# Performance work log

Measured on AMD Instinct MI355X. Metric: run time of the kernel, lower is better.

The kernel has to match this reference:

```python
import jax, jax.numpy as jnp
import numpy as np

NUM_CHANNELS = 512
B_DIM = 64
C_DIM = 16
N = 512
FEAT = NUM_CHANNELS * 4 * 4  # 8192


def setup_inputs() -> dict:
    key = jax.random.key(0)
    k1, k2 = jax.random.split(key)
    inp = jax.random.normal(k1, (N, NUM_CHANNELS, 4, 4), dtype=jnp.float32)
    T = jax.random.normal(k2, (FEAT, B_DIM * C_DIM), dtype=jnp.float32) * 0.1
    return {"inp": inp, "T": T}


def reference(inp, T):
    x = inp.reshape(-1, FEAT)                      # (N, 8192)
    M = (x @ T).reshape(-1, B_DIM, C_DIM)          # (N, B, C)
    # pairwise L1 distance over C: (N, N, B)
    dist = jnp.sum(jnp.abs(M[:, None, :, :] - M[None, :, :, :]), axis=-1)
    o = jnp.sum(jnp.exp(-dist), axis=1)            # (N, B)
    return jnp.concatenate((x, o), axis=1)         # (N, 8192 + B)
```

## Files before the change

### kernel.cpp

```cpp
#include <hip/hip_runtime.h>

#define NROWS 512
#define FEAT  8192
#define BDIM  64
#define CDIM  16
#define MCOLS 1024
#define OUTC  8256
#define KSPLIT 8
#define KCHUNK (FEAT / KSPLIT)
#define MSIZE  (NROWS * MCOLS)

typedef __bf16 bf16x8 __attribute__((ext_vector_type(8)));
typedef float  floatx4 __attribute__((ext_vector_type(4)));

#define AS1 __attribute__((address_space(1)))
#define AS3 __attribute__((address_space(3)))

static __device__ __forceinline__ void gload16(const void* g, void* l) {
    __builtin_amdgcn_global_load_lds((AS1 void*)(g), (AS3 void*)(l), 16, 0, 0);
}

static __device__ __forceinline__ unsigned short f2bf(float f) {
    unsigned int x = __builtin_bit_cast(unsigned int, f);
    unsigned int r = (x + 0x7FFFu + ((x >> 16) & 1u)) >> 16;
    return (unsigned short)r;
}

__global__ __launch_bounds__(512, 2) void k_prep(const float* __restrict__ x,
                                                 const float* __restrict__ T,
                                                 unsigned short* __restrict__ xb,
                                                 unsigned short* __restrict__ Tt,
                                                 float* __restrict__ out) {
    __shared__ __align__(16) float lds[2][64][65];
    int bid = blockIdx.x, t = threadIdx.x;
#pragma unroll
    for (int u = 0; u < 8; ++u) {
        int gid = bid * 4096 + u * 512 + t;
        float4 v = *(const float4*)(x + (size_t)gid * 4);
        ushort4 uu;
        uu.x = f2bf(v.x); uu.y = f2bf(v.y); uu.z = f2bf(v.z); uu.w = f2bf(v.w);
        *(ushort4*)(xb + (size_t)gid * 4) = uu;
        int row = gid >> 11, col4 = gid & 2047;
        *(float4*)(out + (size_t)row * OUTC + col4 * 4) = v;
    }
    int sub = t >> 8, tt = t & 255;
    for (int u = 0; u < 4; ++u) {
        int tile = bid * 8 + u * 2 + sub;
        int kt = tile & 127, nt = tile >> 7;
        __syncthreads();
        int kk = tt >> 2, q = tt & 3;
#pragma unroll
        for (int p = 0; p < 4; ++p) {
            int c4 = q + p * 4;
            float4 v = *(const float4*)(T + (size_t)(kt * 64 + kk) * MCOLS + nt * 64 + c4 * 4);
            lds[sub][kk][c4 * 4 + 0] = v.x; lds[sub][kk][c4 * 4 + 1] = v.y;
            lds[sub][kk][c4 * 4 + 2] = v.z; lds[sub][kk][c4 * 4 + 3] = v.w;
        }
        __syncthreads();
        int nr = tt >> 2, ck = tt & 3;
        unsigned int wv[8];
#pragma unroll
        for (int j = 0; j < 8; ++j) {
            unsigned int lo = f2bf(lds[sub][ck * 16 + j * 2 + 0][nr]);
            unsigned int hi = f2bf(lds[sub][ck * 16 + j * 2 + 1][nr]);
            wv[j] = lo | (hi << 16);
        }
        uint4* dst = (uint4*)(Tt + (size_t)(nt * 64 + nr) * FEAT + kt * 64 + ck * 16);
        dst[0] = make_uint4(wv[0], wv[1], wv[2], wv[3]);
        dst[1] = make_uint4(wv[4], wv[5], wv[6], wv[7]);
    }
}

__global__ __launch_bounds__(256, 2) void k_gemm(const unsigned short* __restrict__ xb,
                                                 const unsigned short* __restrict__ Tt,
                                                 float* __restrict__ Mp) {
    __shared__ __align__(16) unsigned short ldsA[128 * 64];
    __shared__ __align__(16) unsigned short ldsB[64 * 64];
    int bid = blockIdx.x, t = threadIdx.x;
    int mt = bid & 3, nt = (bid >> 2) & 15, ks = bid >> 6;
    int m0 = mt * 128, n0 = nt * 64, kbase = ks * KCHUNK;
    int w = t >> 6, l = t & 63;

    int c  = (l & 3) ^ ((l >> 3) & 3);
    int lr = l >> 2;
    const unsigned short* gA0 = xb + (size_t)(m0 + w * 32 + lr) * FEAT + kbase + c * 8;
    const unsigned short* gA1 = gA0 + (size_t)16 * FEAT;
    const unsigned short* gB0 = Tt + (size_t)(n0 + w * 16 + lr) * FEAT + kbase + c * 8;
    unsigned short* lA00 = ldsA + (4 * w + 0) * 512;
    unsigned short* lA01 = ldsA + (4 * w + 1) * 512;
    unsigned short* lA10 = ldsA + (4 * w + 2) * 512;
    unsigned short* lA11 = ldsA + (4 * w + 3) * 512;
    unsigned short* lB0  = ldsB + (2 * w + 0) * 512;
    unsigned short* lB1  = ldsB + (2 * w + 1) * 512;

    int wr = w >> 1, wc = w & 1, fm = l & 15, fq = l >> 4;
    int fo = fm * 32 + ((fq ^ ((fm >> 1) & 3)) * 8);
    const unsigned short* paB = ldsA + (wr * 8) * 512 + fo;
    const unsigned short* pbB = ldsB + (wc * 4) * 512 + fo;

    floatx4 acc[4][2] = {};

    for (int kk = 0; kk < KCHUNK; kk += 64) {
        __syncthreads();
        gload16(gA0 + kk,      lA00);
        gload16(gA0 + kk + 32, lA01);
        gload16(gA1 + kk,      lA10);
        gload16(gA1 + kk + 32, lA11);
        gload16(gB0 + kk,      lB0);
        gload16(gB0 + kk + 32, lB1);
        __syncthreads();
#pragma unroll
        for (int h = 0; h < 2; ++h) {
            bf16x8 af[4], bfr[2];
#pragma unroll
            for (int a = 0; a < 4; ++a) af[a]  = *(const bf16x8*)(paB + (a * 2 + h) * 512);
#pragma unroll
            for (int b = 0; b < 2; ++b) bfr[b] = *(const bf16x8*)(pbB + (b * 2 + h) * 512);
#pragma unroll
            for (int a = 0; a < 4; ++a)
#pragma unroll
                for (int b = 0; b < 2; ++b)
                    acc[a][b] = __builtin_amdgcn_mfma_f32_16x16x32_bf16(af[a], bfr[b], acc[a][b], 0, 0, 0);
        }
    }

    float* outp = Mp + (size_t)ks * MSIZE;
    int gr0 = m0 + wr * 64, gc0 = n0 + wc * 32;
#pragma unroll
    for (int a = 0; a < 4; ++a)
#pragma unroll
        for (int r = 0; r < 4; ++r) {
            int row = gr0 + a * 16 + fq * 4 + r;
#pragma unroll
            for (int b = 0; b < 2; ++b)
                outp[(size_t)row * MCOLS + gc0 + b * 16 + fm] = acc[a][b][r];
        }
}

__global__ __launch_bounds__(512, 2) void k_pair(const float* __restrict__ Mp,
                                                 float* __restrict__ out) {
    __shared__ float ldsM[NROWS * 20];
    __shared__ float partial[8][64];
    int bid = blockIdx.x, t = threadIdx.x;
    int b = bid & 63, itp = bid >> 6;
#pragma unroll
    for (int p = 0; p < 4; ++p) {
        int idx = t + p * 512;
        int j = idx >> 2, c4 = idx & 3;
        const float* base = Mp + (size_t)j * MCOLS + b * CDIM + c4 * 4;
        float4 s = *(const float4*)base;
#pragma unroll
        for (int k = 1; k < KSPLIT; ++k) {
            float4 v = *(const float4*)(base + (size_t)k * MSIZE);
            s.x += v.x; s.y += v.y; s.z += v.z; s.w += v.w;
        }
        *(float4*)&ldsM[j * 20 + c4 * 4] = s;
    }
    __syncthreads();

    int lane = t & 63, w = t >> 6, g = t >> 8, wg = (t >> 6) & 3;
    int i = (itp * 2 + g) * 64 + lane;
    float mi[CDIM];
#pragma unroll
    for (int cc = 0; cc < CDIM; ++cc) mi[cc] = ldsM[i * 20 + cc];

    float acc = 0.0f;
    for (int jj = wg * 128; jj < wg * 128 + 128; ++jj) {
        float d = 0.0f;
#pragma unroll
        for (int cc = 0; cc < CDIM; ++cc) d += fabsf(mi[cc] - ldsM[jj * 20 + cc]);
        acc += __expf(-d);
    }
    partial[w][lane] = acc;
    __syncthreads();
    if ((t & 255) < 64) {
        int ii = (itp * 2 + g) * 64 + (t & 63);
        float o = partial[g * 4 + 0][t & 63] + partial[g * 4 + 1][t & 63] +
                  partial[g * 4 + 2][t & 63] + partial[g * 4 + 3][t & 63];
        out[(size_t)ii * OUTC + FEAT + b] = o;
    }
}

extern "C" void kernel_launch(void* const* d_in, const int* in_sizes, int n_in,
                              void* d_out, int out_size, void* d_ws, size_t ws_size,
                              hipStream_t stream) {
    const float* x = (const float*)d_in[0];
    const float* T = (const float*)d_in[1];
    float* out = (float*)d_out;

    unsigned short* xb = (unsigned short*)d_ws;
    unsigned short* Tt = (unsigned short*)((char*)d_ws + (8u << 20));
    float*          Mp = (float*)((char*)d_ws + (24u << 20));

    k_prep<<<256, 512, 0, stream>>>(x, T, xb, Tt, out);
    k_gemm<<<512, 256, 0, stream>>>(xb, Tt, Mp);
    k_pair<<<256, 512, 0, stream>>>(Mp, out);
}
```

Baseline: 136.0 us.

## Use packed fp16 L1 distances in pair kernel and split prep into separate blocks

The pairwise kernel now stores the reduced M rows as packed fp16 in shared memory and computes the L1 distance with packed half2 subtract, abs and add. This cuts LDS traffic and ALU work in the O(N^2·B) inner loop. The cost is reduced precision in the distances before exp, which may hurt accuracy. Separately, the prep kernel launches twice as many blocks so x conversion and T transposition run in different blocks instead of sequentially in the same block.

Result: no change. 137.9 us (+1.4%).

```diff
diff --git a/kernel.cpp b/kernel.cpp
--- a/kernel.cpp
+++ b/kernel.cpp
@@ -12,6 +12,7 @@
 
 typedef __bf16 bf16x8 __attribute__((ext_vector_type(8)));
 typedef float  floatx4 __attribute__((ext_vector_type(4)));
+typedef _Float16 half2 __attribute__((ext_vector_type(2)));
 
 #define AS1 __attribute__((address_space(1)))
 #define AS3 __attribute__((address_space(3)))
@@ -24,6 +25,15 @@
     unsigned int x = __builtin_bit_cast(unsigned int, f);
     unsigned int r = (x + 0x7FFFu + ((x >> 16) & 1u)) >> 16;
     return (unsigned short)r;
+}
+
+static __device__ __forceinline__ unsigned int pk2h(float a, float b) {
+    return __builtin_bit_cast(unsigned int, __builtin_amdgcn_cvt_pkrtz(a, b));
+}
+
+static __device__ __forceinline__ half2 absdiff2(unsigned int a, unsigned int b) {
+    half2 d = __builtin_bit_cast(half2, a) - __builtin_bit_cast(half2, b);
+    return __builtin_bit_cast(half2, __builtin_bit_cast(unsigned int, d) & 0x7FFF7FFFu);
 }
 
 __global__ __launch_bounds__(512, 2) void k_prep(const float* __restrict__ x,
@@ -33,41 +43,45 @@
                                                  float* __restrict__ out) {
     __shared__ __align__(16) float lds[2][64][65];
     int bid = blockIdx.x, t = threadIdx.x;
-#pragma unroll
-    for (int u = 0; u < 8; ++u) {
-        int gid = bid * 4096 + u * 512 + t;
-        float4 v = *(const float4*)(x + (size_t)gid * 4);
-        ushort4 uu;
-        uu.x = f2bf(v.x); uu.y = f2bf(v.y); uu.z = f2bf(v.z); uu.w = f2bf(v.w);
-        *(ushort4*)(xb + (size_t)gid * 4) = uu;
-        int row = gid >> 11, col4 = gid & 2047;
-        *(float4*)(out + (size_t)row * OUTC + col4 * 4) = v;
-    }
-    int sub = t >> 8, tt = t & 255;
-    for (int u = 0; u < 4; ++u) {
-        int tile = bid * 8 + u * 2 + sub;
-        int kt = tile & 127, nt = tile >> 7;
-        __syncthreads();
-        int kk = tt >> 2, q = tt & 3;
-#pragma unroll
-        for (int p = 0; p < 4; ++p) {
-            int c4 = q + p * 4;
-            float4 v = *(const float4*)(T + (size_t)(kt * 64 + kk) * MCOLS + nt * 64 + c4 * 4);
-            lds[sub][kk][c4 * 4 + 0] = v.x; lds[sub][kk][c4 * 4 + 1] = v.y;
-            lds[sub][kk][c4 * 4 + 2] = v.z; lds[sub][kk][c4 * 4 + 3] = v.w;
-        }
-        __syncthreads();
-        int nr = tt >> 2, ck = tt & 3;
-        unsigned int wv[8];
-#pragma unroll
-        for (int j = 0; j < 8; ++j) {
-            unsigned int lo = f2bf(lds[sub][ck * 16 + j * 2 + 0][nr]);
-            unsigned int hi = f2bf(lds[sub][ck * 16 + j * 2 + 1][nr]);
-            wv[j] = lo | (hi << 16);
-        }
-        uint4* dst = (uint4*)(Tt + (size_t)(nt * 64 + nr) * FEAT + kt * 64 + ck * 16);
-        dst[0] = make_uint4(wv[0], wv[1], wv[2], wv[3]);
-        dst[1] = make_uint4(wv[4], wv[5], wv[6], wv[7]);
+    if (bid < 256) {
+#pragma unroll
+        for (int u = 0; u < 8; ++u) {
+            int gid = bid * 4096 + u * 512 + t;
+            float4 v = *(const float4*)(x + (size_t)gid * 4);
+            ushort4 uu;
+            uu.x = f2bf(v.x); uu.y = f2bf(v.y); uu.z = f2bf(v.z); uu.w = f2bf(v.w);
+            *(ushort4*)(xb + (size_t)gid * 4) = uu;
+            int row = gid >> 11, col4 = gid & 2047;
+            *(float4*)(out + (size_t)row * OUTC + col4 * 4) = v;
+        }
+    } else {
+        int b2 = bid - 256;
+        int sub = t >> 8, tt = t & 255;
+        for (int u = 0; u < 4; ++u) {
+            int tile = b2 * 8 + u * 2 + sub;
+            int kt = tile & 127, nt = tile >> 7;
+            __syncthreads();
+            int kk = tt >> 2, q = tt & 3;
+#pragma unroll
+            for (int p = 0; p < 4; ++p) {
+                int c4 = q + p * 4;
+                float4 v = *(const float4*)(T + (size_t)(kt * 64 + kk) * MCOLS + nt * 64 + c4 * 4);
+                lds[sub][kk][c4 * 4 + 0] = v.x; lds[sub][kk][c4 * 4 + 1] = v.y;
+                lds[sub][kk][c4 * 4 + 2] = v.z; lds[sub][kk][c4 * 4 + 3] = v.w;
+            }
+            __syncthreads();
+            int nr = tt >> 2, ck = tt & 3;
+            unsigned int wv[8];
+#pragma unroll
+            for (int j = 0; j < 8; ++j) {
+                unsigned int lo = f2bf(lds[sub][ck * 16 + j * 2 + 0][nr]);
+                unsigned int hi = f2bf(lds[sub][ck * 16 + j * 2 + 1][nr]);
+                wv[j] = lo | (hi << 16);
+            }
+            uint4* dst = (uint4*)(Tt + (size_t)(nt * 64 + nr) * FEAT + kt * 64 + ck * 16);
+            dst[0] = make_uint4(wv[0], wv[1], wv[2], wv[3]);
+            dst[1] = make_uint4(wv[4], wv[5], wv[6], wv[7]);
+        }
     }
 }
 
@@ -139,7 +153,7 @@
 
 __global__ __launch_bounds__(512, 2) void k_pair(const float* __restrict__ Mp,
                                                  float* __restrict__ out) {
-    __shared__ float ldsM[NROWS * 20];
+    __shared__ __align__(16) unsigned int ldsMh[NROWS * 12];
     __shared__ float partial[8][64];
     int bid = blockIdx.x, t = threadIdx.x;
     int b = bid & 63, itp = bid >> 6;
@@ -154,21 +168,28 @@
             float4 v = *(const float4*)(base + (size_t)k * MSIZE);
             s.x += v.x; s.y += v.y; s.z += v.z; s.w += v.w;
         }
-        *(float4*)&ldsM[j * 20 + c4 * 4] = s;
+        uint2 wv;
+        wv.x = pk2h(s.x, s.y);
+        wv.y = pk2h(s.z, s.w);
+        *(uint2*)&ldsMh[j * 12 + c4 * 2] = wv;
     }
     __syncthreads();
 
     int lane = t & 63, w = t >> 6, g = t >> 8, wg = (t >> 6) & 3;
     int i = (itp * 2 + g) * 64 + lane;
-    float mi[CDIM];
-#pragma unroll
-    for (int cc = 0; cc < CDIM; ++cc) mi[cc] = ldsM[i * 20 + cc];
+    uint4 miA = *(const uint4*)&ldsMh[i * 12];
+    uint4 miB = *(const uint4*)&ldsMh[i * 12 + 4];
 
     float acc = 0.0f;
     for (int jj = wg * 128; jj < wg * 128 + 128; ++jj) {
-        float d = 0.0f;
-#pragma unroll
-        for (int cc = 0; cc < CDIM; ++cc) d += fabsf(mi[cc] - ldsM[jj * 20 + cc]);
+        uint4 mjA = *(const uint4*)&ldsMh[jj * 12];
+        uint4 mjB = *(const uint4*)&ldsMh[jj * 12 + 4];
+        half2 sA = (absdiff2(miA.x, mjA.x) + absdiff2(miA.y, mjA.y)) +
+                   (absdiff2(miA.z, mjA.z) + absdiff2(miA.w, mjA.w));
+        half2 sB = (absdiff2(miB.x, mjB.x) + absdiff2(miB.y, mjB.y)) +
+                   (absdiff2(miB.z, mjB.z) + absdiff2(miB.w, mjB.w));
+        half2 s = sA + sB;
+        float d = (float)s.x + (float)s.y;
         acc += __expf(-d);
     }
     partial[w][lane] = acc;
@@ -192,7 +213,7 @@
     unsigned short* Tt = (unsigned short*)((char*)d_ws + (8u << 20));
     float*          Mp = (float*)((char*)d_ws + (24u << 20));
 
-    k_prep<<<256, 512, 0, stream>>>(x, T, xb, Tt, out);
+    k_prep<<<512, 512, 0, stream>>>(x, T, xb, Tt, out);
     k_gemm<<<512, 256, 0, stream>>>(xb, Tt, Mp);
     k_pair<<<256, 512, 0, stream>>>(Mp, out);
 }
```
